# Optimization experiments

Hardware: AMD Instinct MI355X
Metric: run time of the kernel (lower is better)

## Reference

```python
import jax, jax.numpy as jnp
import numpy as np

GROUP_SIZES = [16, 16, 16, 16]
K = 2
TEMPERATURE = 1.0
NEG = float(np.finfo(np.float32).min)  # torch.finfo(dtype).min


def setup_inputs() -> dict:
    key = jax.random.key(0)
    k1, k2, k3 = jax.random.split(key, 3)
    B, S, D, E, G = 8, 4096, 1024, 64, len(GROUP_SIZES)
    x = jax.random.normal(k1, (B, S, D), dtype=jnp.float32)
    W_group = jax.random.normal(k2, (G, D), dtype=jnp.float32) * 0.02
    W_expert = jax.random.normal(k3, (E, D), dtype=jnp.float32) * 0.02
    return {"x": x, "W_group": W_group, "W_expert": W_expert}


def reference(x, W_group, W_expert):
    E = W_expert.shape[0]
    # group id of each expert (contiguous ranges) -- static
    expert_group = jnp.asarray(np.repeat(np.arange(len(GROUP_SIZES)), GROUP_SIZES))  # [E]

    # gate logits (no bias), temperature scaling
    expert_logits = jnp.einsum('bsd,ed->bse', x, W_expert) * (1.0 / TEMPERATURE)  # [B,S,E]
    group_logits = jnp.einsum('bsd,gd->bsg', x, W_group)                          # [B,S,G]
    group_probs = jax.nn.softmax(group_logits, axis=-1)
    g_idx = jnp.argmax(group_probs, axis=-1)                                      # [B,S]

    # mask experts outside the selected group's contiguous range
    mask = expert_group[None, None, :] != g_idx[..., None]                        # [B,S,E] bool
    mdt = mask.astype(expert_logits.dtype)
    masked_logits = mdt * NEG + (1.0 - mdt) * expert_logits

    probs_full = jax.nn.softmax(masked_logits, axis=-1)                           # [B,S,E]
    topk_vals, idx = jax.lax.top_k(masked_logits, K)                              # [B,S,K]
    scores = jax.nn.softmax(topk_vals, axis=-1)

    # aux stats (no_grad in original)
    importance = jax.lax.stop_gradient(jnp.mean(probs_full, axis=(0, 1)))         # [E]
    counts = jnp.zeros((E,), probs_full.dtype).at[idx.reshape(-1)].add(1.0)       # [E]
    load = counts / jnp.maximum(jnp.sum(counts), 1.0)
    return (idx, scores, probs_full, importance, load)
```

## Files before the change

kernel.cpp:

```cpp
#include <hip/hip_runtime.h>
#include <math.h>

#define TOKENS   32768
#define DDIM     1024
#define TPB      64
#define NBLOCKS  (TOKENS / TPB)

#define OFF_SCORES 65536
#define OFF_PROBS  131072
#define OFF_IMP    2228224
#define OFF_LOAD   2228288

#define NSLOT 16

typedef __attribute__((ext_vector_type(8))) short  short8;
typedef __attribute__((ext_vector_type(4))) float  f32x4;
typedef __attribute__((ext_vector_type(4))) int    intx4;

__device__ __attribute__((aligned(16))) short wfrag[32 * 5 * 3 * 64 * 8];

__device__ inline void barrier_nodrain() {
  asm volatile("s_waitcnt lgkmcnt(0)" ::: "memory");
  __builtin_amdgcn_sched_barrier(0);
  __builtin_amdgcn_s_barrier();
  __builtin_amdgcn_sched_barrier(0);
}

__device__ inline unsigned rne_hi(float x) {
  unsigned u = __float_as_uint(x);
  unsigned r = u + 0x7fffu + ((u >> 16) & 1u);
  return r & 0xffff0000u;
}

__device__ inline void split3(const float* xv, short8& f1, short8& f2, short8& f3) {
  int o1[4], o2[4], o3[4];
  #pragma unroll
  for (int p = 0; p < 4; ++p) {
    float x0 = xv[2*p], x1 = xv[2*p+1];
    unsigned h0 = rne_hi(x0), h1 = rne_hi(x1);
    o1[p] = (int)((h0 >> 16) | (h1 & 0xffff0000u));
    float r0 = x0 - __uint_as_float(h0);
    float r1 = x1 - __uint_as_float(h1);
    unsigned g0 = rne_hi(r0), g1 = rne_hi(r1);
    o2[p] = (int)((g0 >> 16) | (g1 & 0xffff0000u));
    float s0 = r0 - __uint_as_float(g0);
    float s1 = r1 - __uint_as_float(g1);
    unsigned w0 = rne_hi(s0), w1 = rne_hi(s1);
    o3[p] = (int)((w0 >> 16) | (w1 & 0xffff0000u));
  }
  intx4 t1 = {o1[0], o1[1], o1[2], o1[3]};
  intx4 t2 = {o2[0], o2[1], o2[2], o2[3]};
  intx4 t3 = {o3[0], o3[1], o3[2], o3[3]};
  f1 = __builtin_bit_cast(short8, t1);
  f2 = __builtin_bit_cast(short8, t2);
  f3 = __builtin_bit_cast(short8, t3);
}

__global__ void prep_kernel(const float* __restrict__ Wg, const float* __restrict__ We,
                            float* __restrict__ ws) {
  const int nt   = blockIdx.x >> 5;
  const int ks   = blockIdx.x & 31;
  const int lane = threadIdx.x & 63;
  if (blockIdx.x < 32) ws[blockIdx.x * 64 + lane] = 0.f;
  const int row  = nt * 16 + (lane & 15);
  const int k0   = ks * 32 + (lane >> 4) * 8;
  float xv[8];
  #pragma unroll
  for (int j = 0; j < 8; ++j) {
    float v = 0.f;
    if (row < 64)      v = We[(size_t)row * DDIM + k0 + j];
    else if (row < 68) v = Wg[(size_t)(row - 64) * DDIM + k0 + j];
    xv[j] = v;
  }
  short8 f1, f2, f3;
  split3(xv, f1, f2, f3);
  short8* dst = (short8*)wfrag + (((size_t)ks * 5 + nt) * 3) * 64 + lane;
  dst[0]   = f1;
  dst[64]  = f2;
  dst[128] = f3;
}

__global__ __launch_bounds__(256)
__attribute__((amdgpu_waves_per_eu(2)))
void router_kernel(const float* __restrict__ x,
                   float* __restrict__ out,
                   float* __restrict__ ws) {
  __shared__ __attribute__((aligned(16))) char smem[61440 + 256];
  float*  el     = (float*)smem;
  short8* bstage = (short8*)smem;
  int*    cnt    = (int*)(smem + 61440);
  const int tid    = threadIdx.x;
  const int lane   = tid & 63;
  const int wv     = tid >> 6;
  const int khalf  = wv >> 1;
  const int mhalf  = wv & 1;
  const int quad   = lane >> 4;
  const int m      = lane & 15;
  const int tokblk = blockIdx.x * TPB;

  if (tid < 64) cnt[tid] = 0;

  const float* apb = x + (size_t)(tokblk + mhalf * 32 + m) * DDIM + khalf * 512 + quad * 8;
  const short8* wsrc = (const short8*)wfrag;

  f32x4 ahi[2][5], alo[2][5];
  #pragma unroll
  for (int mt = 0; mt < 2; ++mt)
    #pragma unroll
    for (int nt = 0; nt < 5; ++nt) { ahi[mt][nt] = 0.f; alo[mt][nt] = 0.f; }

  float4 cur[4], nxt[4];
  #pragma unroll
  for (int mt = 0; mt < 2; ++mt) {
    const float* p = apb + (size_t)(mt * 16) * DDIM;
    cur[mt * 2]     = *(const float4*)(p);
    cur[mt * 2 + 1] = *(const float4*)(p + 4);
  }

  {
    short8 breg[8];
    #pragma unroll
    for (int j = 0; j < 8; ++j) {
      const int c = wv + 4 * j;
      if (c < 30) {
        const int ksg = (c < 15) ? 0 : 16;
        const int fr  = (c < 15) ? c : c - 15;
        breg[j] = wsrc[((size_t)ksg * 15 + fr) * 64 + lane];
      }
    }
    #pragma unroll
    for (int j = 0; j < 8; ++j) {
      const int c = wv + 4 * j;
      if (c < 30) bstage[c * 64 + lane] = breg[j];
    }
  }
  barrier_nodrain();

  for (int ks = 0; ks < 16; ++ks) {
    const int pb = ks & 1;
    short8 breg[8];
    if (ks < 15) {
      #pragma unroll
      for (int j = 0; j < 8; ++j) {
        const int c = wv + 4 * j;
        if (c < 30) {
          const int ksg = (c < 15) ? (ks + 1) : (16 + ks + 1);
          const int fr  = (c < 15) ? c : c - 15;
          breg[j] = wsrc[((size_t)ksg * 15 + fr) * 64 + lane];
        }
      }
      #pragma unroll
      for (int mt = 0; mt < 2; ++mt) {
        const float* p = apb + (size_t)(mt * 16) * DDIM + (ks + 1) * 32;
        nxt[mt * 2]     = *(const float4*)(p);
        nxt[mt * 2 + 1] = *(const float4*)(p + 4);
      }
    }
    short8 fa[2][3];
    #pragma unroll
    for (int mt = 0; mt < 2; ++mt) {
      float av[8] = {cur[mt*2].x, cur[mt*2].y, cur[mt*2].z, cur[mt*2].w,
                     cur[mt*2+1].x, cur[mt*2+1].y, cur[mt*2+1].z, cur[mt*2+1].w};
      split3(av, fa[mt][0], fa[mt][1], fa[mt][2]);
    }
    const short8* bbase = &bstage[(size_t)pb * 1920 + (size_t)khalf * 15 * 64 + lane];
    short8 fb0 = bbase[0], fb1 = bbase[64], fb2 = bbase[128];
    #pragma unroll
    for (int nt = 0; nt < 5; ++nt) {
      short8 n0, n1, n2;
      if (nt < 4) {
        n0 = bbase[(nt + 1) * 192];
        n1 = bbase[(nt + 1) * 192 + 64];
        n2 = bbase[(nt + 1) * 192 + 128];
      }
      #pragma unroll
      for (int mt = 0; mt < 2; ++mt) {
        ahi[mt][nt] = __builtin_amdgcn_mfma_f32_16x16x32_bf16(fa[mt][0], fb0, ahi[mt][nt], 0, 0, 0);
        f32x4 c = alo[mt][nt];
        c = __builtin_amdgcn_mfma_f32_16x16x32_bf16(fa[mt][0], fb1, c, 0, 0, 0);
        c = __builtin_amdgcn_mfma_f32_16x16x32_bf16(fa[mt][1], fb0, c, 0, 0, 0);
        c = __builtin_amdgcn_mfma_f32_16x16x32_bf16(fa[mt][1], fb1, c, 0, 0, 0);
        c = __builtin_amdgcn_mfma_f32_16x16x32_bf16(fa[mt][0], fb2, c, 0, 0, 0);
        c = __builtin_amdgcn_mfma_f32_16x16x32_bf16(fa[mt][2], fb0, c, 0, 0, 0);
        c = __builtin_amdgcn_mfma_f32_16x16x32_bf16(fa[mt][1], fb2, c, 0, 0, 0);
        c = __builtin_amdgcn_mfma_f32_16x16x32_bf16(fa[mt][2], fb1, c, 0, 0, 0);
        alo[mt][nt] = c;
      }
      if (nt < 4) { fb0 = n0; fb1 = n1; fb2 = n2; }
    }
    if (ks < 15) {
      #pragma unroll
      for (int j = 0; j < 8; ++j) {
        const int c = wv + 4 * j;
        if (c < 30) bstage[(size_t)(pb ^ 1) * 1920 + c * 64 + lane] = breg[j];
      }
      barrier_nodrain();
      #pragma unroll
      for (int i = 0; i < 4; ++i) cur[i] = nxt[i];
    }
  }

  if (khalf == 1) {
    #pragma unroll
    for (int mt = 0; mt < 2; ++mt)
      #pragma unroll
      for (int nt = 0; nt < 5; ++nt)
        #pragma unroll
        for (int r = 0; r < 4; ++r)
          el[(mhalf * 32 + mt * 16 + quad * 4 + r) * 88 + nt * 16 + m] = ahi[mt][nt][r] + alo[mt][nt][r];
  }
  __syncthreads();
  if (khalf == 0) {
    #pragma unroll
    for (int mt = 0; mt < 2; ++mt)
      #pragma unroll
      for (int nt = 0; nt < 5; ++nt)
        #pragma unroll
        for (int r = 0; r < 4; ++r) {
          const int idx = (mhalf * 32 + mt * 16 + quad * 4 + r) * 88 + nt * 16 + m;
          el[idx] += ahi[mt][nt][r] + alo[mt][nt][r];
        }
  }
  __syncthreads();

  if (tid < TPB) {
    const int t = tid;
    float* row = el + t * 88;
    const float g0 = row[64], g1 = row[65], g2 = row[66], g3 = row[67];
    int g = 0; float gb = g0;
    if (g1 > gb) { g = 1; gb = g1; }
    if (g2 > gb) { g = 2; gb = g2; }
    if (g3 > gb) { g = 3; gb = g3; }
    const int base = g << 4;
    float l[16];
    #pragma unroll
    for (int e = 0; e < 16; ++e) l[e] = row[base + e];
    int i1 = 0; float v1 = l[0];
    #pragma unroll
    for (int e = 1; e < 16; ++e) if (l[e] > v1) { i1 = e; v1 = l[e]; }
    int i2 = -1; float v2 = 0.f;
    #pragma unroll
    for (int e = 0; e < 16; ++e) {
      if (e == i1) continue;
      if (i2 < 0 || l[e] > v2) { i2 = e; v2 = l[e]; }
    }
    float pr[16]; float s = 0.f;
    #pragma unroll
    for (int e = 0; e < 16; ++e) { pr[e] = expf(l[e] - v1); s += pr[e]; }
    const float inv = 1.f / s;
    #pragma unroll
    for (int c = 0; c < 64; ++c) row[c] = 0.f;
    #pragma unroll
    for (int e = 0; e < 16; ++e) row[base + e] = pr[e] * inv;
    const size_t T = (size_t)tokblk + t;
    out[2*T]     = (float)(base + i1);
    out[2*T + 1] = (float)(base + i2);
    const float e2 = expf(v2 - v1);
    const float si = 1.f / (1.f + e2);
    out[OFF_SCORES + 2*T]     = si;
    out[OFF_SCORES + 2*T + 1] = e2 * si;
    atomicAdd(&cnt[base + i1], 1);
    atomicAdd(&cnt[base + i2], 1);
  }
  __syncthreads();

  for (int i = tid; i < TPB * 64; i += 256) {
    const int t = i >> 6, c = i & 63;
    out[OFF_PROBS + (((size_t)(tokblk + t)) << 6) + c] = el[t * 88 + c];
  }
  if (tid < 64) {
    const int e = tid;
    float s = 0.f;
    #pragma unroll 4
    for (int t = 0; t < TPB; ++t) s += el[t * 88 + e];
    const int slot = (blockIdx.x & (NSLOT - 1)) * 128;
    atomicAdd(&ws[slot + e], s);
    atomicAdd(&ws[slot + 64 + e], (float)cnt[e]);
  }
}

__global__ void finalize_kernel(const float* __restrict__ ws, float* __restrict__ out) {
  const int e = threadIdx.x;
  if (e < 64) {
    float imp = 0.f, cf = 0.f;
    #pragma unroll
    for (int s = 0; s < NSLOT; ++s) {
      imp += ws[s * 128 + e];
      cf  += ws[s * 128 + 64 + e];
    }
    out[OFF_IMP  + e] = imp * (1.0f / 32768.0f);
    out[OFF_LOAD + e] = cf  * (1.0f / 65536.0f);
  }
}

extern "C" void kernel_launch(void* const* d_in, const int* in_sizes, int n_in,
                              void* d_out, int out_size, void* d_ws, size_t ws_size,
                              hipStream_t stream) {
  (void)in_sizes; (void)n_in; (void)out_size; (void)ws_size;
  const float* x  = (const float*)d_in[0];
  const float* Wg = (const float*)d_in[1];
  const float* We = (const float*)d_in[2];
  float* out = (float*)d_out;
  float* ws  = (float*)d_ws;
  hipLaunchKernelGGL(prep_kernel, dim3(160), dim3(64), 0, stream, Wg, We, ws);
  hipLaunchKernelGGL(router_kernel, dim3(NBLOCKS), dim3(256), 0, stream, x, out, ws);
  hipLaunchKernelGGL(finalize_kernel, dim3(1), dim3(64), 0, stream, ws, out);
}
```

Measured before the change: 208.9 us.

## Prefetch x two k-steps ahead and fuse finalize into router via last-block atomic

```diff
diff --git a/kernel.cpp b/kernel.cpp
--- a/kernel.cpp
+++ b/kernel.cpp
@@ -62,6 +62,7 @@
   const int ks   = blockIdx.x & 31;
   const int lane = threadIdx.x & 63;
   if (blockIdx.x < 32) ws[blockIdx.x * 64 + lane] = 0.f;
+  if (blockIdx.x == 0 && threadIdx.x == 0) ((unsigned*)ws)[2048] = 0u;
   const int row  = nt * 16 + (lane & 15);
   const int k0   = ks * 32 + (lane >> 4) * 8;
   float xv[8];
@@ -85,7 +86,7 @@
 void router_kernel(const float* __restrict__ x,
                    float* __restrict__ out,
                    float* __restrict__ ws) {
-  __shared__ __attribute__((aligned(16))) char smem[61440 + 256];
+  __shared__ __attribute__((aligned(16))) char smem[61440 + 384];
   float*  el     = (float*)smem;
   short8* bstage = (short8*)smem;
   int*    cnt    = (int*)(smem + 61440);
@@ -109,12 +110,14 @@
     #pragma unroll
     for (int nt = 0; nt < 5; ++nt) { ahi[mt][nt] = 0.f; alo[mt][nt] = 0.f; }
 
-  float4 cur[4], nxt[4];
+  float4 cur[4], nx1[4], nx2[4];
   #pragma unroll
   for (int mt = 0; mt < 2; ++mt) {
     const float* p = apb + (size_t)(mt * 16) * DDIM;
     cur[mt * 2]     = *(const float4*)(p);
     cur[mt * 2 + 1] = *(const float4*)(p + 4);
+    nx1[mt * 2]     = *(const float4*)(p + 32);
+    nx1[mt * 2 + 1] = *(const float4*)(p + 36);
   }
 
   {
@@ -149,11 +152,13 @@
           breg[j] = wsrc[((size_t)ksg * 15 + fr) * 64 + lane];
         }
       }
+    }
+    if (ks < 14) {
       #pragma unroll
       for (int mt = 0; mt < 2; ++mt) {
-        const float* p = apb + (size_t)(mt * 16) * DDIM + (ks + 1) * 32;
-        nxt[mt * 2]     = *(const float4*)(p);
-        nxt[mt * 2 + 1] = *(const float4*)(p + 4);
+        const float* p = apb + (size_t)(mt * 16) * DDIM + (ks + 2) * 32;
+        nx2[mt * 2]     = *(const float4*)(p);
+        nx2[mt * 2 + 1] = *(const float4*)(p + 4);
       }
     }
     short8 fa[2][3];
@@ -196,7 +201,7 @@
       }
       barrier_nodrain();
       #pragma unroll
-      for (int i = 0; i < 4; ++i) cur[i] = nxt[i];
+      for (int i = 0; i < 4; ++i) { cur[i] = nx1[i]; nx1[i] = nx2[i]; }
     }
   }
 
@@ -277,16 +282,22 @@
     atomicAdd(&ws[slot + e], s);
     atomicAdd(&ws[slot + 64 + e], (float)cnt[e]);
   }
-}
-
-__global__ void finalize_kernel(const float* __restrict__ ws, float* __restrict__ out) {
-  const int e = threadIdx.x;
-  if (e < 64) {
+
+  __syncthreads();
+  if (tid == 0) {
+    __threadfence();
+    unsigned prev = __hip_atomic_fetch_add((unsigned*)(ws + 2048), 1u,
+                                           __ATOMIC_ACQ_REL, __HIP_MEMORY_SCOPE_AGENT);
+    cnt[64] = (prev == (unsigned)(NBLOCKS - 1)) ? 1 : 0;
+  }
+  __syncthreads();
+  if (cnt[64] && tid < 64) {
+    const int e = tid;
     float imp = 0.f, cf = 0.f;
     #pragma unroll
     for (int s = 0; s < NSLOT; ++s) {
-      imp += ws[s * 128 + e];
-      cf  += ws[s * 128 + 64 + e];
+      imp += __hip_atomic_load(&ws[s * 128 + e],      __ATOMIC_RELAXED, __HIP_MEMORY_SCOPE_AGENT);
+      cf  += __hip_atomic_load(&ws[s * 128 + 64 + e], __ATOMIC_RELAXED, __HIP_MEMORY_SCOPE_AGENT);
     }
     out[OFF_IMP  + e] = imp * (1.0f / 32768.0f);
     out[OFF_LOAD + e] = cf  * (1.0f / 65536.0f);
@@ -304,5 +315,4 @@
   float* ws  = (float*)d_ws;
   hipLaunchKernelGGL(prep_kernel, dim3(160), dim3(64), 0, stream, Wg, We, ws);
   hipLaunchKernelGGL(router_kernel, dim3(NBLOCKS), dim3(256), 0, stream, x, out, ws);
-  hipLaunchKernelGGL(finalize_kernel, dim3(1), dim3(64), 0, stream, ws, out);
-}
+}
```

Measured after the change: 227.7 us. +9.0%, slower.
